# Performance work log

Hardware: AMD Instinct MI355X
Metric: run time of the kernel (lower is better)

## Reference

```python
import jax, jax.numpy as jnp
import numpy as np
import math

B, N, D, H = 4, 1024, 256, 8  # batch, points, dim_V, heads
DH = D // H                   # per-head dim = 32
INF = jnp.float32(1e38)


def setup_inputs() -> dict:
    key = jax.random.key(0)
    ks = jax.random.split(key, 16)
    s = 0.02
    inp = {
        "X_lift": jax.random.normal(ks[0], (B, N, 3), jnp.float32),
        "Y_lift": jax.random.normal(ks[1], (B, N, D), jnp.float32),
        "X_pairs": jax.random.normal(ks[2], (B, N, N, 3), jnp.float32),
        "presence_q": (jax.random.uniform(ks[3], (B, N)) < 0.9).astype(jnp.float32),
        "presence_k": (jax.random.uniform(ks[4], (B, N)) < 0.9).astype(jnp.float32),
        # projection weights, stored [in, out]
        "Wq": jax.random.normal(ks[5], (D, D), jnp.float32) * s,
        "bq": jnp.zeros((D,), jnp.float32),
        "Wk": jax.random.normal(ks[6], (D, D), jnp.float32) * s,
        "bk": jnp.zeros((D,), jnp.float32),
        "Wv": jax.random.normal(ks[7], (D, D), jnp.float32) * s,
        "bv": jnp.zeros((D,), jnp.float32),
        "Wo": jax.random.normal(ks[8], (D, D), jnp.float32) * s,
        "bo": jnp.zeros((D,), jnp.float32),
        # per-head location-bias MLPs: Linear(3,3) -> ReLU -> Linear(3,1)
        "Wg1": jax.random.normal(ks[9], (H, 3, 3), jnp.float32) * 0.5,
        "bg1": jnp.zeros((H, 3), jnp.float32),
        "wg2": jax.random.normal(ks[10], (H, 3), jnp.float32) * 0.5,
        "bg2": jnp.zeros((H,), jnp.float32),
    }
    return inp


def reference(X_lift, Y_lift, X_pairs, presence_q, presence_k,
              Wq, bq, Wk, bk, Wv, bv, Wo, bo, Wg1, bg1, wg2, bg2):
    # X_lift is unused by the original forward (keys=queries=values=Y_lift)
    Q = Y_lift @ Wq + bq          # [B,N,D]
    K = Y_lift @ Wk + bk
    V = Y_lift @ Wv + bv

    # split into heads, head-major layout [H,B,N,DH]
    Qh = Q.reshape(B, N, H, DH).transpose(2, 0, 1, 3)
    Kh = K.reshape(B, N, H, DH).transpose(2, 0, 1, 3)
    Vh = V.reshape(B, N, H, DH).transpose(2, 0, 1, 3)

    content = jnp.einsum('hbnd,hbmd->hbnm', Qh, Kh) / math.sqrt(D)

    # per-head pairwise location bias MLP on X_pairs [B,N,N,3]
    hid = jax.nn.relu(jnp.einsum('bnmc,hcd->hbnmd', X_pairs, Wg1)
                      + bg1[:, None, None, None, :])       # [H,B,N,N,3]
    loc = jnp.einsum('hbnmd,hd->hbnm', hid, wg2) + bg2[:, None, None, None]

    logits = content + loc                                  # [H,B,N,N]

    pq = presence_q[None, :, :, None]                       # [1,B,N,1]
    logits = pq * logits - (1.0 - pq) * INF
    pk = presence_k[None, :, None, :]                       # [1,B,1,N]
    logits = pk * logits - (1.0 - pk) * INF

    A = jax.nn.softmax(logits, axis=-1)                     # [H,B,N,N]
    Oh = jnp.einsum('hbnm,hbmd->hbnd', A, Vh)               # [H,B,N,DH]
    O = V + Oh.transpose(1, 2, 0, 3).reshape(B, N, D)       # residual on values
    O = O + jax.nn.relu(O @ Wo + bo)
    return O
```

## Files before the change

### kernel.cpp

```cpp
#include <hip/hip_runtime.h>
#include <hip/hip_bf16.h>
#include <math.h>

typedef __bf16 bf16;
typedef __bf16 bf16x4 __attribute__((ext_vector_type(4)));
typedef __bf16 bf16x8 __attribute__((ext_vector_type(8)));
typedef float f32x2 __attribute__((ext_vector_type(2)));
typedef float f32x4 __attribute__((ext_vector_type(4)));

#define NB 4
#define NN 1024
#define ND 256
#define NH 8
#define INFV 1e38f
#define RTHR2 11.5f
#define LOG2E 1.44269504f
#define ZSPLIT 4

__device__ __forceinline__ f32x4 mfma16(bf16x8 a, bf16x8 b, f32x4 c) {
    return __builtin_amdgcn_mfma_f32_16x16x32_bf16(a, b, c, 0, 0, 0);
}
__device__ __forceinline__ f32x2 sp2(float v) { return f32x2{v, v}; }
__device__ __forceinline__ f32x2 fma2(f32x2 a, float b, f32x2 c) {
    return __builtin_elementwise_fma(a, sp2(b), c);
}
__device__ __forceinline__ float rfl(float x) {
    return __int_as_float(__builtin_amdgcn_readfirstlane(__float_as_int(x)));
}

template<int MODE>
__global__ __launch_bounds__(256)
void gemm_k(const float* __restrict__ A,
            const float* __restrict__ W0, const float* __restrict__ b0,
            const float* __restrict__ W1, const float* __restrict__ b1,
            const float* __restrict__ W2, const float* __restrict__ b2,
            float* __restrict__ Fo2, bf16* __restrict__ G0,
            bf16* __restrict__ G1, bf16* __restrict__ Gt,
            float* __restrict__ Fo1, const float* __restrict__ addsrc)
{
    const int z = blockIdx.z;
    const float* W    = (z == 0) ? W0 : (z == 1) ? W1 : W2;
    const float* bias = (z == 0) ? b0 : (z == 1) ? b1 : b2;

    const int brow = blockIdx.x * 64;
    const int bcol = blockIdx.y * 64;
    const int t    = threadIdx.x;
    const int lane = t & 63;
    const int w    = t >> 6;
    const int wr   = w >> 1, wc = w & 1;
    const int g    = lane >> 4;
    const int l16  = lane & 15;

    __shared__ bf16 As[64][40];
    __shared__ bf16 Wt[64][40];

    f32x4 acc[2][2];
    #pragma unroll
    for (int i = 0; i < 2; ++i)
        #pragma unroll
        for (int j = 0; j < 2; ++j) acc[i][j] = f32x4{0.f, 0.f, 0.f, 0.f};

    const int ar = t >> 2, aj = (t & 3) * 8;
    const int wcid = t & 63, wk = (t >> 6) * 8;

    for (int k0 = 0; k0 < 256; k0 += 32) {
        {
            const float4 v0 = *(const float4*)&A[(size_t)(brow + ar)*ND + k0 + aj];
            const float4 v1 = *(const float4*)&A[(size_t)(brow + ar)*ND + k0 + aj + 4];
            bf16x8 w8 = { (bf16)v0.x, (bf16)v0.y, (bf16)v0.z, (bf16)v0.w,
                          (bf16)v1.x, (bf16)v1.y, (bf16)v1.z, (bf16)v1.w };
            *(bf16x8*)&As[ar][aj] = w8;
        }
        {
            bf16x8 w8;
            #pragma unroll
            for (int p = 0; p < 8; ++p)
                w8[p] = (bf16)W[(size_t)(k0 + wk + p)*ND + bcol + wcid];
            *(bf16x8*)&Wt[wcid][wk] = w8;
        }
        __syncthreads();

        bf16x8 af[2], bfj[2];
        #pragma unroll
        for (int i = 0; i < 2; ++i) af[i]  = *(const bf16x8*)&As[wr*32 + i*16 + l16][8*g];
        #pragma unroll
        for (int j = 0; j < 2; ++j) bfj[j] = *(const bf16x8*)&Wt[wc*32 + j*16 + l16][8*g];
        #pragma unroll
        for (int j = 0; j < 2; ++j)
            #pragma unroll
            for (int i = 0; i < 2; ++i) acc[i][j] = mfma16(af[i], bfj[j], acc[i][j]);
        __syncthreads();
    }

    #pragma unroll
    for (int j = 0; j < 2; ++j) {
        const int col = bcol + wc*32 + j*16 + l16;
        const float bj = bias[col];
        #pragma unroll
        for (int i = 0; i < 2; ++i) {
            const int row0 = brow + wr*32 + i*16 + 4*g;
            if (MODE == 1) {
                #pragma unroll
                for (int r = 0; r < 4; ++r) {
                    const size_t idx = (size_t)(row0 + r)*ND + col;
                    Fo1[idx] = addsrc[idx] + fmaxf(acc[i][j][r] + bj, 0.f);
                }
            } else if (z < 2) {
                bf16* Go = (z == 0) ? G0 : G1;
                #pragma unroll
                for (int r = 0; r < 4; ++r)
                    Go[(size_t)(row0 + r)*ND + col] = (bf16)(acc[i][j][r] + bj);
            } else {
                float vv[4];
                #pragma unroll
                for (int r = 0; r < 4; ++r) {
                    vv[r] = acc[i][j][r] + bj;
                    Fo2[(size_t)(row0 + r)*ND + col] = vv[r];
                }
                const int b2 = row0 >> 10;
                const int n0 = row0 & 1023;
                bf16x4 tv = { (bf16)vv[0], (bf16)vv[1], (bf16)vv[2], (bf16)vv[3] };
                *(bf16x4*)&Gt[((size_t)b2*ND + col)*NN + n0] = tv;
            }
        }
    }
}

__global__ __launch_bounds__(256, 4)
void attn_k(const bf16* __restrict__ Qb, const bf16* __restrict__ Kb,
            const bf16* __restrict__ Vt, const float* __restrict__ Xpg,
            const float* __restrict__ prq, const float* __restrict__ prk,
            const float* __restrict__ Wg1, const float* __restrict__ bg1,
            const float* __restrict__ wg2, const float* __restrict__ bg2,
            float* __restrict__ Ohp, float* __restrict__ ml)
{
    const int yb   = blockIdx.y;
    const int b    = yb >> 1;
    const int hg   = yb & 1;
    const int q0   = blockIdx.x * 16;
    const int z    = blockIdx.z;
    const int mb0  = z * (NN/ZSPLIT);
    const int t    = threadIdx.x;
    const int w    = t >> 6;
    const int h    = hg*4 + w;
    const int lane = t & 63;
    const int g    = lane >> 4;
    const int l16  = lane & 15;
    const int NT   = NN/ZSPLIT/32;

    __shared__ float Xps[2][16*132];
    __shared__ bf16  Ps[4][16][40];

    float g1[3][3], gb1[3], g2v[3], gb2v;
    #pragma unroll
    for (int c = 0; c < 3; ++c)
        #pragma unroll
        for (int d = 0; d < 3; ++d) g1[c][d] = rfl(Wg1[(h*3 + c)*3 + d]);
    #pragma unroll
    for (int d = 0; d < 3; ++d) {
        gb1[d] = rfl(bg1[h*3 + d]);
        g2v[d] = rfl(wg2[h*3 + d]*LOG2E);
    }
    gb2v = rfl(bg2[h]*LOG2E);
    const float sscale = 0.0625f * LOG2E;

    const bf16x8 qf = *(const bf16x8*)&Qb[((size_t)b*NN + q0 + l16)*ND + h*32 + 8*g];

    bool okq[4];
    #pragma unroll
    for (int r = 0; r < 4; ++r)
        okq[r] = prq[b*NN + q0 + 4*g + r] > 0.5f;

    float m_run[4], l_run[4];
    f32x4 oh[2];
    #pragma unroll
    for (int r = 0; r < 4; ++r) { m_run[r] = -INFINITY; l_run[r] = 0.f; }
    oh[0] = f32x4{0.f,0.f,0.f,0.f};
    oh[1] = f32x4{0.f,0.f,0.f,0.f};

    const bf16*  kp0 = &Kb[((size_t)b*NN + mb0 + l16)*ND + h*32 + 8*g];
    const bf16*  kp1 = kp0 + (size_t)16*ND;
    const bf16*  vp0 = &Vt[((size_t)b*ND + h*32 + l16)*NN + mb0 + 8*g];
    const bf16*  vp1 = vp0 + (size_t)16*NN;
    const int    xq  = t >> 5, xm = t & 31;
    const float* xppA = &Xpg[(((size_t)b*NN + q0 + xq)*NN + mb0 + xm)*3];
    const float* xppB = &Xpg[(((size_t)b*NN + q0 + xq + 8)*NN + mb0 + xm)*3];
    const float* pkp  = &prk[(size_t)b*NN + mb0 + l16];

    bf16x8 kf0 = *(const bf16x8*)kp0;
    bf16x8 kf1 = *(const bf16x8*)kp1;
    bf16x8 vf0 = *(const bf16x8*)vp0;
    bf16x8 vf1 = *(const bf16x8*)vp1;
    float xxA = xppA[0], xyA = xppA[1], xzA = xppA[2];
    float xxB = xppB[0], xyB = xppB[1], xzB = xppB[2];
    float pk0 = pkp[0], pk1 = pkp[16];
    {
        float* dA = &Xps[0][xq*132 + xm*4];
        dA[0] = xxA; dA[1] = xyA; dA[2] = xzA;
        float* dB = &Xps[0][(xq + 8)*132 + xm*4];
        dB[0] = xxB; dB[1] = xyB; dB[2] = xzB;
    }
    __syncthreads();

    for (int it = 0; it < NT; ++it) {
        const int cur = it & 1;

        bf16x8 kn0, kn1, vn0, vn1;
        float  xnxA, xnyA, xnzA, xnxB, xnyB, xnzB, pn0, pn1;
        if (it + 1 < NT) {
            const int off = (it + 1) * 32;
            kn0 = *(const bf16x8*)(kp0 + (size_t)off*ND);
            kn1 = *(const bf16x8*)(kp1 + (size_t)off*ND);
            vn0 = *(const bf16x8*)(vp0 + off);
            vn1 = *(const bf16x8*)(vp1 + off);
            xnxA = xppA[(size_t)off*3];
            xnyA = xppA[(size_t)off*3 + 1];
            xnzA = xppA[(size_t)off*3 + 2];
            xnxB = xppB[(size_t)off*3];
            xnyB = xppB[(size_t)off*3 + 1];
            xnzB = xppB[(size_t)off*3 + 2];
            pn0 = pkp[off]; pn1 = pkp[off + 16];
        }

        const f32x4 zero = {0.f,0.f,0.f,0.f};
        f32x4 s[2];
        s[0] = mfma16(qf, kf0, zero);
        s[1] = mfma16(qf, kf1, zero);

        const bool okk0 = pk0 > 0.5f;
        const bool okk1 = pk1 > 0.5f;

        float lv[2][4];
        #pragma unroll
        for (int mg = 0; mg < 2; ++mg) {
            const bool okkm = mg ? okk1 : okk0;
            const int m = mg*16 + l16;
            #pragma unroll
            for (int rp = 0; rp < 2; ++rp) {
                const int q = 4*g + 2*rp;
                const float4 xa = *(const float4*)&Xps[cur][q*132 + m*4];
                const float4 xb = *(const float4*)&Xps[cur][(q+1)*132 + m*4];
                const f32x2 vx = {xa.x, xb.x};
                const f32x2 vy = {xa.y, xb.y};
                const f32x2 vz = {xa.z, xb.z};
                f32x2 h0 = fma2(vz, g1[2][0], fma2(vy, g1[1][0], fma2(vx, g1[0][0], sp2(gb1[0]))));
                f32x2 h1 = fma2(vz, g1[2][1], fma2(vy, g1[1][1], fma2(vx, g1[0][1], sp2(gb1[1]))));
                f32x2 h2 = fma2(vz, g1[2][2], fma2(vy, g1[1][2], fma2(vx, g1[0][2], sp2(gb1[2]))));
                const f32x2 zz = {0.f, 0.f};
                h0 = __builtin_elementwise_max(h0, zz);
                h1 = __builtin_elementwise_max(h1, zz);
                h2 = __builtin_elementwise_max(h2, zz);
                f32x2 loc = fma2(h2, g2v[2], fma2(h1, g2v[1], fma2(h0, g2v[0], sp2(gb2v))));
                const f32x2 s2 = { s[mg][2*rp], s[mg][2*rp+1] };
                const f32x2 y = fma2(s2, sscale, loc);
                lv[mg][2*rp]   = (okq[2*rp]   && okkm) ? y.x : -INFV;
                lv[mg][2*rp+1] = (okq[2*rp+1] && okkm) ? y.y : -INFV;
            }
        }

        float pm[4];
        #pragma unroll
        for (int r = 0; r < 4; ++r) pm[r] = fmaxf(lv[0][r], lv[1][r]);
        const bool cond = (pm[0] <= m_run[0] + RTHR2) && (pm[1] <= m_run[1] + RTHR2)
                       && (pm[2] <= m_run[2] + RTHR2) && (pm[3] <= m_run[3] + RTHR2);
        if (!__all((int)cond)) {
            #pragma unroll
            for (int r = 0; r < 4; ++r) {
                float mx = pm[r];
                mx = fmaxf(mx, __shfl_xor(mx, 1));
                mx = fmaxf(mx, __shfl_xor(mx, 2));
                mx = fmaxf(mx, __shfl_xor(mx, 4));
                mx = fmaxf(mx, __shfl_xor(mx, 8));
                const float mnew = fmaxf(m_run[r], mx);
                const float corr = exp2f(m_run[r] - mnew);
                l_run[r] *= corr;
                oh[0][r] *= corr;
                oh[1][r] *= corr;
                m_run[r] = mnew;
            }
        }
        #pragma unroll
        for (int r = 0; r < 4; ++r) {
            const float p0 = exp2f(lv[0][r] - m_run[r]);
            const float p1 = exp2f(lv[1][r] - m_run[r]);
            Ps[w][4*g + r][l16]      = (bf16)p0;
            Ps[w][4*g + r][16 + l16] = (bf16)p1;
            l_run[r] += p0 + p1;
        }

        asm volatile("s_waitcnt lgkmcnt(0)" ::: "memory");
        __builtin_amdgcn_sched_barrier(0);

        const bf16x8 pf = *(const bf16x8*)&Ps[w][l16][8*g];
        oh[0] = mfma16(pf, vf0, oh[0]);
        oh[1] = mfma16(pf, vf1, oh[1]);

        if (it + 1 < NT) {
            float* dA = &Xps[cur ^ 1][xq*132 + xm*4];
            dA[0] = xnxA; dA[1] = xnyA; dA[2] = xnzA;
            float* dB = &Xps[cur ^ 1][(xq + 8)*132 + xm*4];
            dB[0] = xnxB; dB[1] = xnyB; dB[2] = xnzB;
            kf0 = kn0; kf1 = kn1; vf0 = vn0; vf1 = vn1;
            pk0 = pn0; pk1 = pn1;
        }
        __syncthreads();
    }

    #pragma unroll
    for (int r = 0; r < 4; ++r) {
        float ls = l_run[r];
        ls += __shfl_xor(ls, 1);
        ls += __shfl_xor(ls, 2);
        ls += __shfl_xor(ls, 4);
        ls += __shfl_xor(ls, 8);
        const int n = q0 + 4*g + r;
        #pragma unroll
        for (int dg = 0; dg < 2; ++dg) {
            const int col = h*32 + dg*16 + l16;
            Ohp[(((size_t)z*NB + b)*NN + n)*ND + col] = oh[dg][r];
        }
        if (l16 == 0) {
            const size_t mi = ((((size_t)z*NB + b)*NN + n)*NH + h)*2;
            ml[mi]   = m_run[r];
            ml[mi+1] = ls;
        }
    }
}

__global__ __launch_bounds__(256)
void comb_k(const float* __restrict__ Ohp, const float* __restrict__ ml,
            const float* __restrict__ Vf, float* __restrict__ O1)
{
    const int idx = blockIdx.x * 256 + threadIdx.x;
    const int dq = idx & 63;
    const int bn = idx >> 6;
    const int d0 = dq * 4;
    const int h  = dq >> 3;

    const size_t base = ((size_t)bn*NH + h)*2;
    const size_t zstr = (size_t)NB*NN*NH*2;
    float mz[ZSPLIT], lz[ZSPLIT];
    float M = -INFINITY;
    #pragma unroll
    for (int zi = 0; zi < ZSPLIT; ++zi) {
        mz[zi] = ml[base + zi*zstr];
        lz[zi] = ml[base + zi*zstr + 1];
        M = fmaxf(M, mz[zi]);
    }
    float wz[ZSPLIT], den = 0.f;
    #pragma unroll
    for (int zi = 0; zi < ZSPLIT; ++zi) {
        wz[zi] = exp2f(mz[zi] - M);
        den = fmaf(lz[zi], wz[zi], den);
    }
    const float inv = 1.f / den;

    const size_t e = (size_t)bn*ND + d0;
    f32x4 num = {0.f,0.f,0.f,0.f};
    #pragma unroll
    for (int zi = 0; zi < ZSPLIT; ++zi) {
        const f32x4 o = *(const f32x4*)&Ohp[e + (size_t)zi*NB*NN*ND];
        #pragma unroll
        for (int r = 0; r < 4; ++r) num[r] = fmaf(o[r], wz[zi], num[r]);
    }
    const f32x4 vf = *(const f32x4*)&Vf[e];
    f32x4 out;
    #pragma unroll
    for (int r = 0; r < 4; ++r) out[r] = vf[r] + num[r]*inv;
    *(f32x4*)&O1[e] = out;
}

extern "C" void kernel_launch(void* const* d_in, const int* in_sizes, int n_in,
                              void* d_out, int out_size, void* d_ws, size_t ws_size,
                              hipStream_t stream)
{
    const float* Y   = (const float*)d_in[1];
    const float* Xp  = (const float*)d_in[2];
    const float* prq = (const float*)d_in[3];
    const float* prk = (const float*)d_in[4];
    const float* Wq  = (const float*)d_in[5];
    const float* bq  = (const float*)d_in[6];
    const float* Wk  = (const float*)d_in[7];
    const float* bk  = (const float*)d_in[8];
    const float* Wv  = (const float*)d_in[9];
    const float* bv  = (const float*)d_in[10];
    const float* Wo  = (const float*)d_in[11];
    const float* bo  = (const float*)d_in[12];
    const float* Wg1 = (const float*)d_in[13];
    const float* bg1 = (const float*)d_in[14];
    const float* wg2 = (const float*)d_in[15];
    const float* bg2 = (const float*)d_in[16];
    float* out = (float*)d_out;

    const size_t BND = (size_t)NB * NN * ND;
    float* Vf  = (float*)d_ws;
    float* Ohp = Vf + BND;
    float* ml  = Ohp + (size_t)ZSPLIT*BND;
    bf16*  Qb  = (bf16*)(ml + (size_t)ZSPLIT*NB*NN*NH*2);
    bf16*  Kb  = Qb + BND;
    bf16*  Vt  = Kb + BND;
    float* O1  = (float*)Qb;

    gemm_k<0><<<dim3(64, 4, 3), 256, 0, stream>>>(
        Y, Wq, bq, Wk, bk, Wv, bv,
        Vf, Qb, Kb, Vt, nullptr, nullptr);

    attn_k<<<dim3(NN/16, NB*2, ZSPLIT), 256, 0, stream>>>(
        Qb, Kb, Vt, Xp, prq, prk, Wg1, bg1, wg2, bg2, Ohp, ml);

    comb_k<<<dim3(1024), 256, 0, stream>>>(Ohp, ml, Vf, O1);

    gemm_k<1><<<dim3(64, 4, 1), 256, 0, stream>>>(
        O1, Wo, bo, Wo, bo, Wo, bo,
        nullptr, nullptr, nullptr, nullptr, out, O1);
}
```

Measured before the change: 72.15 us.

## Process 32 queries per attention block to reuse K/V fragments

Each attention block now handles two 16-query sub-tiles, so every K and V fragment loaded from global memory feeds two MFMA sets instead of one. This halves the grid's x dimension and removes the V register double-buffering; V and presence_k are now loaded at the top of each iteration rather than prefetched one iteration ahead. Shared memory and register use per block roughly double, and the launch bound drops to 2 blocks per CU, which lowers occupancy and may expose the V load latency. The X_pairs traffic is unchanged, since each block still streams its own query rows.

```diff
diff --git a/kernel.cpp b/kernel.cpp
--- a/kernel.cpp
+++ b/kernel.cpp
@@ -126,7 +126,7 @@
     }
 }
 
-__global__ __launch_bounds__(256, 4)
+__global__ __launch_bounds__(256, 2)
 void attn_k(const bf16* __restrict__ Qb, const bf16* __restrict__ Kb,
             const bf16* __restrict__ Vt, const float* __restrict__ Xpg,
             const float* __restrict__ prq, const float* __restrict__ prk,
@@ -137,7 +137,7 @@
     const int yb   = blockIdx.y;
     const int b    = yb >> 1;
     const int hg   = yb & 1;
-    const int q0   = blockIdx.x * 16;
+    const int q0   = blockIdx.x * 32;
     const int z    = blockIdx.z;
     const int mb0  = z * (NN/ZSPLIT);
     const int t    = threadIdx.x;
@@ -148,8 +148,8 @@
     const int l16  = lane & 15;
     const int NT   = NN/ZSPLIT/32;
 
-    __shared__ float Xps[2][16*132];
-    __shared__ bf16  Ps[4][16][40];
+    __shared__ float Xps[2][32*132];
+    __shared__ bf16  Ps[4][32][40];
 
     float g1[3][3], gb1[3], g2v[3], gb2v;
     #pragma unroll
@@ -164,165 +164,210 @@
     gb2v = rfl(bg2[h]*LOG2E);
     const float sscale = 0.0625f * LOG2E;
 
-    const bf16x8 qf = *(const bf16x8*)&Qb[((size_t)b*NN + q0 + l16)*ND + h*32 + 8*g];
-
-    bool okq[4];
-    #pragma unroll
-    for (int r = 0; r < 4; ++r)
-        okq[r] = prq[b*NN + q0 + 4*g + r] > 0.5f;
-
-    float m_run[4], l_run[4];
-    f32x4 oh[2];
-    #pragma unroll
-    for (int r = 0; r < 4; ++r) { m_run[r] = -INFINITY; l_run[r] = 0.f; }
-    oh[0] = f32x4{0.f,0.f,0.f,0.f};
-    oh[1] = f32x4{0.f,0.f,0.f,0.f};
+    const bf16x8 qfA = *(const bf16x8*)&Qb[((size_t)b*NN + q0 + l16)*ND + h*32 + 8*g];
+    const bf16x8 qfB = *(const bf16x8*)&Qb[((size_t)b*NN + q0 + 16 + l16)*ND + h*32 + 8*g];
+
+    bool okqA[4], okqB[4];
+    #pragma unroll
+    for (int r = 0; r < 4; ++r) {
+        okqA[r] = prq[b*NN + q0 + 4*g + r] > 0.5f;
+        okqB[r] = prq[b*NN + q0 + 16 + 4*g + r] > 0.5f;
+    }
+
+    float mA[4], lA[4], mB[4], lB[4];
+    f32x4 ohA[2], ohB[2];
+    #pragma unroll
+    for (int r = 0; r < 4; ++r) { mA[r] = -INFINITY; lA[r] = 0.f; mB[r] = -INFINITY; lB[r] = 0.f; }
+    ohA[0] = f32x4{0.f,0.f,0.f,0.f}; ohA[1] = f32x4{0.f,0.f,0.f,0.f};
+    ohB[0] = f32x4{0.f,0.f,0.f,0.f}; ohB[1] = f32x4{0.f,0.f,0.f,0.f};
 
     const bf16*  kp0 = &Kb[((size_t)b*NN + mb0 + l16)*ND + h*32 + 8*g];
     const bf16*  kp1 = kp0 + (size_t)16*ND;
     const bf16*  vp0 = &Vt[((size_t)b*ND + h*32 + l16)*NN + mb0 + 8*g];
     const bf16*  vp1 = vp0 + (size_t)16*NN;
     const int    xq  = t >> 5, xm = t & 31;
-    const float* xppA = &Xpg[(((size_t)b*NN + q0 + xq)*NN + mb0 + xm)*3];
-    const float* xppB = &Xpg[(((size_t)b*NN + q0 + xq + 8)*NN + mb0 + xm)*3];
+    const float* xpp0 = &Xpg[(((size_t)b*NN + q0 + xq     )*NN + mb0 + xm)*3];
+    const float* xpp1 = &Xpg[(((size_t)b*NN + q0 + xq +  8)*NN + mb0 + xm)*3];
+    const float* xpp2 = &Xpg[(((size_t)b*NN + q0 + xq + 16)*NN + mb0 + xm)*3];
+    const float* xpp3 = &Xpg[(((size_t)b*NN + q0 + xq + 24)*NN + mb0 + xm)*3];
     const float* pkp  = &prk[(size_t)b*NN + mb0 + l16];
 
     bf16x8 kf0 = *(const bf16x8*)kp0;
     bf16x8 kf1 = *(const bf16x8*)kp1;
-    bf16x8 vf0 = *(const bf16x8*)vp0;
-    bf16x8 vf1 = *(const bf16x8*)vp1;
-    float xxA = xppA[0], xyA = xppA[1], xzA = xppA[2];
-    float xxB = xppB[0], xyB = xppB[1], xzB = xppB[2];
-    float pk0 = pkp[0], pk1 = pkp[16];
     {
-        float* dA = &Xps[0][xq*132 + xm*4];
-        dA[0] = xxA; dA[1] = xyA; dA[2] = xzA;
-        float* dB = &Xps[0][(xq + 8)*132 + xm*4];
-        dB[0] = xxB; dB[1] = xyB; dB[2] = xzB;
+        float x0x = xpp0[0], x0y = xpp0[1], x0z = xpp0[2];
+        float x1x = xpp1[0], x1y = xpp1[1], x1z = xpp1[2];
+        float x2x = xpp2[0], x2y = xpp2[1], x2z = xpp2[2];
+        float x3x = xpp3[0], x3y = xpp3[1], x3z = xpp3[2];
+        float* d0 = &Xps[0][(xq     )*132 + xm*4]; d0[0]=x0x; d0[1]=x0y; d0[2]=x0z;
+        float* d1 = &Xps[0][(xq +  8)*132 + xm*4]; d1[0]=x1x; d1[1]=x1y; d1[2]=x1z;
+        float* d2 = &Xps[0][(xq + 16)*132 + xm*4]; d2[0]=x2x; d2[1]=x2y; d2[2]=x2z;
+        float* d3 = &Xps[0][(xq + 24)*132 + xm*4]; d3[0]=x3x; d3[1]=x3y; d3[2]=x3z;
     }
     __syncthreads();
 
+    #pragma unroll 1
     for (int it = 0; it < NT; ++it) {
         const int cur = it & 1;
-
-        bf16x8 kn0, kn1, vn0, vn1;
-        float  xnxA, xnyA, xnzA, xnxB, xnyB, xnzB, pn0, pn1;
+        const int m0  = it * 32;
+
+        const bf16x8 vf0 = *(const bf16x8*)(vp0 + m0);
+        const bf16x8 vf1 = *(const bf16x8*)(vp1 + m0);
+        const float pk0 = pkp[m0], pk1 = pkp[m0 + 16];
+
+        bf16x8 kn0, kn1;
+        float xn0x, xn0y, xn0z, xn1x, xn1y, xn1z;
+        float xn2x, xn2y, xn2z, xn3x, xn3y, xn3z;
         if (it + 1 < NT) {
-            const int off = (it + 1) * 32;
+            const int off = m0 + 32;
             kn0 = *(const bf16x8*)(kp0 + (size_t)off*ND);
             kn1 = *(const bf16x8*)(kp1 + (size_t)off*ND);
-            vn0 = *(const bf16x8*)(vp0 + off);
-            vn1 = *(const bf16x8*)(vp1 + off);
-            xnxA = xppA[(size_t)off*3];
-            xnyA = xppA[(size_t)off*3 + 1];
-            xnzA = xppA[(size_t)off*3 + 2];
-            xnxB = xppB[(size_t)off*3];
-            xnyB = xppB[(size_t)off*3 + 1];
-            xnzB = xppB[(size_t)off*3 + 2];
-            pn0 = pkp[off]; pn1 = pkp[off + 16];
+            const size_t o3 = (size_t)off*3;
+            xn0x = xpp0[o3]; xn0y = xpp0[o3+1]; xn0z = xpp0[o3+2];
+            xn1x = xpp1[o3]; xn1y = xpp1[o3+1]; xn1z = xpp1[o3+2];
+            xn2x = xpp2[o3]; xn2y = xpp2[o3+1]; xn2z = xpp2[o3+2];
+            xn3x = xpp3[o3]; xn3y = xpp3[o3+1]; xn3z = xpp3[o3+2];
         }
 
         const f32x4 zero = {0.f,0.f,0.f,0.f};
-        f32x4 s[2];
-        s[0] = mfma16(qf, kf0, zero);
-        s[1] = mfma16(qf, kf1, zero);
+        f32x4 sA[2], sB[2];
+        sA[0] = mfma16(qfA, kf0, zero);
+        sA[1] = mfma16(qfA, kf1, zero);
+        sB[0] = mfma16(qfB, kf0, zero);
+        sB[1] = mfma16(qfB, kf1, zero);
 
         const bool okk0 = pk0 > 0.5f;
         const bool okk1 = pk1 > 0.5f;
 
-        float lv[2][4];
-        #pragma unroll
-        for (int mg = 0; mg < 2; ++mg) {
-            const bool okkm = mg ? okk1 : okk0;
-            const int m = mg*16 + l16;
+        float lvA[2][4], lvB[2][4];
+        #pragma unroll
+        for (int half = 0; half < 2; ++half) {
+            float (*lv)[4] = half ? lvB : lvA;
+            const bool* okq = half ? okqB : okqA;
+            const int qbase = half*16 + 4*g;
             #pragma unroll
-            for (int rp = 0; rp < 2; ++rp) {
-                const int q = 4*g + 2*rp;
-                const float4 xa = *(const float4*)&Xps[cur][q*132 + m*4];
-                const float4 xb = *(const float4*)&Xps[cur][(q+1)*132 + m*4];
-                const f32x2 vx = {xa.x, xb.x};
-                const f32x2 vy = {xa.y, xb.y};
-                const f32x2 vz = {xa.z, xb.z};
-                f32x2 h0 = fma2(vz, g1[2][0], fma2(vy, g1[1][0], fma2(vx, g1[0][0], sp2(gb1[0]))));
-                f32x2 h1 = fma2(vz, g1[2][1], fma2(vy, g1[1][1], fma2(vx, g1[0][1], sp2(gb1[1]))));
-                f32x2 h2 = fma2(vz, g1[2][2], fma2(vy, g1[1][2], fma2(vx, g1[0][2], sp2(gb1[2]))));
-                const f32x2 zz = {0.f, 0.f};
-                h0 = __builtin_elementwise_max(h0, zz);
-                h1 = __builtin_elementwise_max(h1, zz);
-                h2 = __builtin_elementwise_max(h2, zz);
-                f32x2 loc = fma2(h2, g2v[2], fma2(h1, g2v[1], fma2(h0, g2v[0], sp2(gb2v))));
-                const f32x2 s2 = { s[mg][2*rp], s[mg][2*rp+1] };
-                const f32x2 y = fma2(s2, sscale, loc);
-                lv[mg][2*rp]   = (okq[2*rp]   && okkm) ? y.x : -INFV;
-                lv[mg][2*rp+1] = (okq[2*rp+1] && okkm) ? y.y : -INFV;
+            for (int mg = 0; mg < 2; ++mg) {
+                const bool okkm = mg ? okk1 : okk0;
+                const int m = mg*16 + l16;
+                #pragma unroll
+                for (int rp = 0; rp < 2; ++rp) {
+                    const int q = qbase + 2*rp;
+                    const float4 xa = *(const float4*)&Xps[cur][q*132 + m*4];
+                    const float4 xb = *(const float4*)&Xps[cur][(q+1)*132 + m*4];
+                    const f32x2 vx = {xa.x, xb.x};
+                    const f32x2 vy = {xa.y, xb.y};
+                    const f32x2 vz = {xa.z, xb.z};
+                    f32x2 h0 = fma2(vz, g1[2][0], fma2(vy, g1[1][0], fma2(vx, g1[0][0], sp2(gb1[0]))));
+                    f32x2 h1 = fma2(vz, g1[2][1], fma2(vy, g1[1][1], fma2(vx, g1[0][1], sp2(gb1[1]))));
+                    f32x2 h2 = fma2(vz, g1[2][2], fma2(vy, g1[1][2], fma2(vx, g1[0][2], sp2(gb1[2]))));
+                    const f32x2 zz = {0.f, 0.f};
+                    h0 = __builtin_elementwise_max(h0, zz);
+                    h1 = __builtin_elementwise_max(h1, zz);
+                    h2 = __builtin_elementwise_max(h2, zz);
+                    f32x2 loc = fma2(h2, g2v[2], fma2(h1, g2v[1], fma2(h0, g2v[0], sp2(gb2v))));
+                    const f32x2 sv = half ? f32x2{ sB[mg][2*rp], sB[mg][2*rp+1] }
+                                          : f32x2{ sA[mg][2*rp], sA[mg][2*rp+1] };
+                    const f32x2 y = fma2(sv, sscale, loc);
+                    lv[mg][2*rp]   = (okq[2*rp]   && okkm) ? y.x : -INFV;
+                    lv[mg][2*rp+1] = (okq[2*rp+1] && okkm) ? y.y : -INFV;
+                }
             }
         }
 
-        float pm[4];
-        #pragma unroll
-        for (int r = 0; r < 4; ++r) pm[r] = fmaxf(lv[0][r], lv[1][r]);
-        const bool cond = (pm[0] <= m_run[0] + RTHR2) && (pm[1] <= m_run[1] + RTHR2)
-                       && (pm[2] <= m_run[2] + RTHR2) && (pm[3] <= m_run[3] + RTHR2);
+        float pmA[4], pmB[4];
+        #pragma unroll
+        for (int r = 0; r < 4; ++r) {
+            pmA[r] = fmaxf(lvA[0][r], lvA[1][r]);
+            pmB[r] = fmaxf(lvB[0][r], lvB[1][r]);
+        }
+        const bool cond = (pmA[0] <= mA[0] + RTHR2) && (pmA[1] <= mA[1] + RTHR2)
+                       && (pmA[2] <= mA[2] + RTHR2) && (pmA[3] <= mA[3] + RTHR2)
+                       && (pmB[0] <= mB[0] + RTHR2) && (pmB[1] <= mB[1] + RTHR2)
+                       && (pmB[2] <= mB[2] + RTHR2) && (pmB[3] <= mB[3] + RTHR2);
         if (!__all((int)cond)) {
             #pragma unroll
             for (int r = 0; r < 4; ++r) {
-                float mx = pm[r];
+                float mx = pmA[r];
                 mx = fmaxf(mx, __shfl_xor(mx, 1));
                 mx = fmaxf(mx, __shfl_xor(mx, 2));
                 mx = fmaxf(mx, __shfl_xor(mx, 4));
                 mx = fmaxf(mx, __shfl_xor(mx, 8));
-                const float mnew = fmaxf(m_run[r], mx);
-                const float corr = exp2f(m_run[r] - mnew);
-                l_run[r] *= corr;
-                oh[0][r] *= corr;
-                oh[1][r] *= corr;
-                m_run[r] = mnew;
+                const float mnew = fmaxf(mA[r], mx);
+                const float corr = exp2f(mA[r] - mnew);
+                lA[r] *= corr; ohA[0][r] *= corr; ohA[1][r] *= corr;
+                mA[r] = mnew;
+                float my = pmB[r];
+                my = fmaxf(my, __shfl_xor(my, 1));
+                my = fmaxf(my, __shfl_xor(my, 2));
+                my = fmaxf(my, __shfl_xor(my, 4));
+                my = fmaxf(my, __shfl_xor(my, 8));
+                const float mnewB = fmaxf(mB[r], my);
+                const float corrB = exp2f(mB[r] - mnewB);
+                lB[r] *= corrB; ohB[0][r] *= corrB; ohB[1][r] *= corrB;
+                mB[r] = mnewB;
             }
         }
         #pragma unroll
         for (int r = 0; r < 4; ++r) {
-            const float p0 = exp2f(lv[0][r] - m_run[r]);
-            const float p1 = exp2f(lv[1][r] - m_run[r]);
-            Ps[w][4*g + r][l16]      = (bf16)p0;
-            Ps[w][4*g + r][16 + l16] = (bf16)p1;
-            l_run[r] += p0 + p1;
+            const float pa0 = exp2f(lvA[0][r] - mA[r]);
+            const float pa1 = exp2f(lvA[1][r] - mA[r]);
+            Ps[w][4*g + r][l16]      = (bf16)pa0;
+            Ps[w][4*g + r][16 + l16] = (bf16)pa1;
+            lA[r] += pa0 + pa1;
+            const float pb0 = exp2f(lvB[0][r] - mB[r]);
+            const float pb1 = exp2f(lvB[1][r] - mB[r]);
+            Ps[w][16 + 4*g + r][l16]      = (bf16)pb0;
+            Ps[w][16 + 4*g + r][16 + l16] = (bf16)pb1;
+            lB[r] += pb0 + pb1;
         }
 
         asm volatile("s_waitcnt lgkmcnt(0)" ::: "memory");
         __builtin_amdgcn_sched_barrier(0);
 
-        const bf16x8 pf = *(const bf16x8*)&Ps[w][l16][8*g];
-        oh[0] = mfma16(pf, vf0, oh[0]);
-        oh[1] = mfma16(pf, vf1, oh[1]);
+        const bf16x8 pfA = *(const bf16x8*)&Ps[w][l16][8*g];
+        const bf16x8 pfB = *(const bf16x8*)&Ps[w][16 + l16][8*g];
+        ohA[0] = mfma16(pfA, vf0, ohA[0]);
+        ohA[1] = mfma16(pfA, vf1, ohA[1]);
+        ohB[0] = mfma16(pfB, vf0, ohB[0]);
+        ohB[1] = mfma16(pfB, vf1, ohB[1]);
 
         if (it + 1 < NT) {
-            float* dA = &Xps[cur ^ 1][xq*132 + xm*4];
-            dA[0] = xnxA; dA[1] = xnyA; dA[2] = xnzA;
-            float* dB = &Xps[cur ^ 1][(xq + 8)*132 + xm*4];
-            dB[0] = xnxB; dB[1] = xnyB; dB[2] = xnzB;
-            kf0 = kn0; kf1 = kn1; vf0 = vn0; vf1 = vn1;
-            pk0 = pn0; pk1 = pn1;
+            float* d0 = &Xps[cur ^ 1][(xq     )*132 + xm*4]; d0[0]=xn0x; d0[1]=xn0y; d0[2]=xn0z;
+            float* d1 = &Xps[cur ^ 1][(xq +  8)*132 + xm*4]; d1[0]=xn1x; d1[1]=xn1y; d1[2]=xn1z;
+            float* d2 = &Xps[cur ^ 1][(xq + 16)*132 + xm*4]; d2[0]=xn2x; d2[1]=xn2y; d2[2]=xn2z;
+            float* d3 = &Xps[cur ^ 1][(xq + 24)*132 + xm*4]; d3[0]=xn3x; d3[1]=xn3y; d3[2]=xn3z;
+            kf0 = kn0; kf1 = kn1;
         }
         __syncthreads();
     }
 
     #pragma unroll
     for (int r = 0; r < 4; ++r) {
-        float ls = l_run[r];
-        ls += __shfl_xor(ls, 1);
-        ls += __shfl_xor(ls, 2);
-        ls += __shfl_xor(ls, 4);
-        ls += __shfl_xor(ls, 8);
-        const int n = q0 + 4*g + r;
+        float lsA = lA[r];
+        lsA += __shfl_xor(lsA, 1);
+        lsA += __shfl_xor(lsA, 2);
+        lsA += __shfl_xor(lsA, 4);
+        lsA += __shfl_xor(lsA, 8);
+        float lsB = lB[r];
+        lsB += __shfl_xor(lsB, 1);
+        lsB += __shfl_xor(lsB, 2);
+        lsB += __shfl_xor(lsB, 4);
+        lsB += __shfl_xor(lsB, 8);
+        const int nA = q0 + 4*g + r;
+        const int nB = q0 + 16 + 4*g + r;
         #pragma unroll
         for (int dg = 0; dg < 2; ++dg) {
             const int col = h*32 + dg*16 + l16;
-            Ohp[(((size_t)z*NB + b)*NN + n)*ND + col] = oh[dg][r];
+            Ohp[(((size_t)z*NB + b)*NN + nA)*ND + col] = ohA[dg][r];
+            Ohp[(((size_t)z*NB + b)*NN + nB)*ND + col] = ohB[dg][r];
         }
         if (l16 == 0) {
-            const size_t mi = ((((size_t)z*NB + b)*NN + n)*NH + h)*2;
-            ml[mi]   = m_run[r];
-            ml[mi+1] = ls;
+            const size_t miA = ((((size_t)z*NB + b)*NN + nA)*NH + h)*2;
+            ml[miA]   = mA[r];
+            ml[miA+1] = lsA;
+            const size_t miB = ((((size_t)z*NB + b)*NN + nB)*NH + h)*2;
+            ml[miB]   = mB[r];
+            ml[miB+1] = lsB;
         }
     }
 }
@@ -405,7 +450,7 @@
         Y, Wq, bq, Wk, bk, Wv, bv,
         Vf, Qb, Kb, Vt, nullptr, nullptr);
 
-    attn_k<<<dim3(NN/16, NB*2, ZSPLIT), 256, 0, stream>>>(
+    attn_k<<<dim3(NN/32, NB*2, ZSPLIT), 256, 0, stream>>>(
         Qb, Kb, Vt, Xp, prq, prk, Wg1, bg1, wg2, bg2, Ohp, ml);
 
     comb_k<<<dim3(1024), 256, 0, stream>>>(Ohp, ml, Vf, O1);
```

New measurement: 73.31 us. About the same (+1.6%).
